# Performance work log

Measured on AMD Instinct MI355X. Metric: run time of the kernel, lower is better.

Reference implementation:

```python
import jax, jax.numpy as jnp
import numpy as np

N, E, D, H, O = 50000, 600000, 128, 128, 64


def _glorot(key, shape):
    fan_in, fan_out = shape[-1], shape[0]
    lim = (6.0 / (fan_in + fan_out)) ** 0.5
    return jax.random.uniform(key, shape, jnp.float32, -lim, lim)


def setup_inputs() -> dict:
    key = jax.random.key(0)
    ks = jax.random.split(key, 20)
    inp = {
        'x': jax.random.normal(ks[0], (N, D), dtype=jnp.float32),
        'edge_index': jax.random.randint(ks[1], (2, E), 0, N, dtype=jnp.int32),
        # FastLocalConv params
        'fl_W': _glorot(ks[2], (H, D)),
        'fl_b': jnp.zeros((H,), jnp.float32),
        'fl_att': _glorot(ks[3], (1, H)),
        # GIN layer 1 MLP: Linear(H,H) -> ReLU -> Linear(H,H)
        'g1_W1': _glorot(ks[4], (H, H)), 'g1_b1': jnp.zeros((H,), jnp.float32),
        'g1_W2': _glorot(ks[5], (H, H)), 'g1_b2': jnp.zeros((H,), jnp.float32),
        # GIN layer 2 MLP
        'g2_W1': _glorot(ks[6], (H, H)), 'g2_b1': jnp.zeros((H,), jnp.float32),
        'g2_W2': _glorot(ks[7], (H, H)), 'g2_b2': jnp.zeros((H,), jnp.float32),
        # output head
        'out_W': _glorot(ks[8], (O, H)), 'out_b': jnp.zeros((O,), jnp.float32),
    }
    return inp


def _fast_local(x, edge_index, W, b, att):
    # add self loops
    loops = jnp.arange(N, dtype=edge_index.dtype)
    row = jnp.concatenate([edge_index[0], loops])
    col = jnp.concatenate([edge_index[1], loops])
    h = x @ W.T + b                                   # [N,H]
    alpha = jax.nn.leaky_relu((h[row] * att[0]).sum(-1), 0.2)  # [E+N]
    # scatter-softmax grouped by source node (row), as in original code
    m = jax.ops.segment_max(alpha, row, num_segments=N)
    ea = jnp.exp(alpha - m[row])
    s = jax.ops.segment_sum(ea, row, num_segments=N)
    a = ea / s[row]
    # aggr='add' into target nodes (col), message = alpha * x_j (x_j = h[row])
    return jax.ops.segment_sum(a[:, None] * h[row], col, num_segments=N)


def _gin(h, edge_index, W1, b1, W2, b2):
    # GINConv (eps=0): mlp(x + sum_{j in N(i)} x_j), no self loops
    agg = jax.ops.segment_sum(h[edge_index[0]], edge_index[1], num_segments=N)
    z = h + agg
    z = jax.nn.relu(z @ W1.T + b1)
    return z @ W2.T + b2


def reference(x, edge_index, fl_W, fl_b, fl_att,
              g1_W1, g1_b1, g1_W2, g1_b2,
              g2_W1, g2_b1, g2_W2, g2_b2,
              out_W, out_b):
    h = _fast_local(x, edge_index, fl_W, fl_b, fl_att)
    h = jax.nn.relu(h)  # (dropout is eval no-op)
    h = jax.nn.relu(_gin(h, edge_index, g1_W1, g1_b1, g1_W2, g1_b2))
    h = jax.nn.relu(_gin(h, edge_index, g2_W1, g2_b1, g2_W2, g2_b2))
    logits = h @ out_W.T + out_b
    return jax.nn.log_softmax(logits, axis=1)
```

## Files before the change

### kernel.cpp

```cpp
#include <hip/hip_runtime.h>
#include <stdint.h>

typedef __attribute__((ext_vector_type(8))) short short8;
typedef __attribute__((ext_vector_type(4))) float floatx4;

#define HB 64
#define NMAX 50000
#define HW 12500

__device__ inline unsigned short f2bf(float f) {
  union { float f; unsigned int u; } v; v.f = f;
  unsigned int u = v.u;
  unsigned int r = (u + 0x7FFFu + ((u >> 16) & 1u)) >> 16;
  return (unsigned short)r;
}
__device__ inline unsigned int pk2(float a, float b) {
  return (unsigned int)f2bf(a) | ((unsigned int)f2bf(b) << 16);
}
template <bool RELU>
__device__ inline void acc8(uint4 u, float* a) {
  float f0 = __uint_as_float(u.x << 16), f1 = __uint_as_float(u.x & 0xffff0000u);
  float f2 = __uint_as_float(u.y << 16), f3 = __uint_as_float(u.y & 0xffff0000u);
  float f4 = __uint_as_float(u.z << 16), f5 = __uint_as_float(u.z & 0xffff0000u);
  float f6 = __uint_as_float(u.w << 16), f7 = __uint_as_float(u.w & 0xffff0000u);
  if (RELU) {
    f0 = fmaxf(f0, 0.f); f1 = fmaxf(f1, 0.f); f2 = fmaxf(f2, 0.f); f3 = fmaxf(f3, 0.f);
    f4 = fmaxf(f4, 0.f); f5 = fmaxf(f5, 0.f); f6 = fmaxf(f6, 0.f); f7 = fmaxf(f7, 0.f);
  }
  a[0] += f0; a[1] += f1; a[2] += f2; a[3] += f3;
  a[4] += f4; a[5] += f5; a[6] += f6; a[7] += f7;
}
__device__ inline uint4 pk8(const float* a) {
  uint4 p;
  p.x = pk2(a[0], a[1]); p.y = pk2(a[2], a[3]);
  p.z = pk2(a[4], a[5]); p.w = pk2(a[6], a[7]);
  return p;
}

__global__ __launch_bounds__(1024) void k_hist(const int* __restrict__ esrc,
                                               const int* __restrict__ edst,
                                               int E, int per,
                                               unsigned int* __restrict__ pAll) {
  __shared__ unsigned int h[HW];
  for (int i = threadIdx.x; i < HW; i += 1024) h[i] = 0;
  __syncthreads();
  const int* idx = blockIdx.y ? esrc : edst;
  int s = blockIdx.x * per, e = min(E, s + per);
  for (int j = s + threadIdx.x; j < e; j += 1024) {
    unsigned int d = (unsigned int)idx[j];
    atomicAdd(&h[d >> 2], 1u << ((d & 3) * 8));
  }
  __syncthreads();
  unsigned int* p = pAll + ((size_t)blockIdx.y * HB + blockIdx.x) * HW;
  for (int i = threadIdx.x; i < HW; i += 1024) p[i] = h[i];
}

__global__ __launch_bounds__(256) void k_reduce(unsigned int* __restrict__ pAll,
                                                int* __restrict__ deg,
                                                float* __restrict__ invc, int N) {
  int w = blockIdx.x * 256 + threadIdx.x;
  if (w >= HW) return;
  unsigned int* pd = pAll + w;
  const unsigned int* ps = pAll + (size_t)HB * HW + w;
  unsigned int r0 = 0, r1 = 0, r2 = 0, r3 = 0;
  for (int b = 0; b < HB; ++b) {
    unsigned int v = pd[(size_t)b * HW];
    pd[(size_t)b * HW] = r0 | (r1 << 8) | (r2 << 16) | (r3 << 24);
    r0 += v & 255u; r1 += (v >> 8) & 255u; r2 += (v >> 16) & 255u; r3 += v >> 24;
  }
  unsigned int s0 = 0, s1 = 0, s2 = 0, s3 = 0;
  for (int b = 0; b < HB; ++b) {
    unsigned int v = ps[(size_t)b * HW];
    s0 += v & 255u; s1 += (v >> 8) & 255u; s2 += (v >> 16) & 255u; s3 += v >> 24;
  }
  int n0 = 4 * w;
  unsigned int rr[4] = {r0, r1, r2, r3}, ss[4] = {s0, s1, s2, s3};
#pragma unroll
  for (int c = 0; c < 4; ++c) {
    if (n0 + c < N) {
      deg[n0 + c] = (int)rr[c];
      invc[n0 + c] = 1.0f / (1.0f + (float)ss[c]);
    }
  }
}

__global__ __launch_bounds__(1024) void k_scan_local(const int* __restrict__ deg,
                                                     int* __restrict__ off,
                                                     int* __restrict__ bsum, int N) {
  __shared__ int sb[1024];
  int tid = threadIdx.x;
  int i = blockIdx.x * 1024 + tid;
  int v = (i < N) ? deg[i] : 0;
  sb[tid] = v;
  __syncthreads();
  for (int d = 1; d < 1024; d <<= 1) {
    int t = (tid >= d) ? sb[tid - d] : 0;
    __syncthreads();
    sb[tid] += t;
    __syncthreads();
  }
  if (i < N) off[i] = sb[tid] - v;
  if (tid == 1023) bsum[blockIdx.x] = sb[1023];
}

__global__ __launch_bounds__(256) void k_scan_fix(int* off, const int* __restrict__ bsum,
                                                  int N, int E) {
  int i = blockIdx.x * 256 + threadIdx.x;
  if (i >= N) return;
  int nb = i >> 10;
  int s = 0;
  for (int c = 0; c < nb; ++c) s += bsum[c];
  off[i] += s;
  if (i == 0) off[N] = E;
}

__global__ __launch_bounds__(1024) void k_fill2(const int* __restrict__ esrc,
                                                const int* __restrict__ edst,
                                                int E, int per,
                                                const unsigned int* __restrict__ pAll,
                                                const int* __restrict__ off,
                                                int* __restrict__ srcs) {
  __shared__ unsigned int rk[HW];
  for (int i = threadIdx.x; i < HW; i += 1024) rk[i] = 0;
  __syncthreads();
  const unsigned int* slab = pAll + (size_t)blockIdx.x * HW;
  int s = blockIdx.x * per, e = min(E, s + per);
  for (int j = s + threadIdx.x; j < e; j += 1024) {
    unsigned int d = (unsigned int)edst[j];
    int sh = (d & 3) * 8;
    unsigned int rank = (atomicAdd(&rk[d >> 2], 1u << sh) >> sh) & 255u;
    unsigned int base = (slab[d >> 2] >> sh) & 255u;
    srcs[off[d] + (int)base + (int)rank] = esrc[j];
  }
}

__global__ __launch_bounds__(256) void k_gemm_fl(const float* __restrict__ in,
                                                 const float* __restrict__ W,
                                                 const float* __restrict__ bias,
                                                 const float* __restrict__ scale,
                                                 unsigned short* __restrict__ out, int N) {
  __shared__ unsigned short sx[64 * 136];
  __shared__ unsigned short sw[128 * 136];
  const int tid = threadIdx.x;
  const int nb = blockIdx.x * 64;

  for (int i = tid; i < 128 * 32; i += 256) {
    int h = i >> 5, k4 = i & 31;
    float4 wv = ((const float4*)W)[i];
    *(uint2*)&sw[h * 136 + k4 * 4] = make_uint2(pk2(wv.x, wv.y), pk2(wv.z, wv.w));
  }
  for (int i = tid; i < 64 * 32; i += 256) {
    int n = i >> 5, k4 = i & 31;
    int gn = nb + n;
    float4 xv;
    if (gn < N) xv = ((const float4*)in)[(size_t)gn * 32 + k4];
    else { xv.x = 0.f; xv.y = 0.f; xv.z = 0.f; xv.w = 0.f; }
    *(uint2*)&sx[n * 136 + k4 * 4] = make_uint2(pk2(xv.x, xv.y), pk2(xv.z, xv.w));
  }
  __syncthreads();

  const int wave = tid >> 6, lane = tid & 63;
  const int quad = lane >> 4, lq = lane & 15;
  floatx4 acc[8];
#pragma unroll
  for (int t = 0; t < 8; ++t) acc[t] = (floatx4){0.f, 0.f, 0.f, 0.f};
  const int arow = (wave * 16 + lq) * 136;
#pragma unroll
  for (int kt = 0; kt < 4; ++kt) {
    short8 a = *(const short8*)&sx[arow + kt * 32 + quad * 8];
#pragma unroll
    for (int t = 0; t < 8; ++t) {
      short8 b = *(const short8*)&sw[(t * 16 + lq) * 136 + kt * 32 + quad * 8];
      acc[t] = __builtin_amdgcn_mfma_f32_16x16x32_bf16(a, b, acc[t], 0, 0, 0);
    }
  }
#pragma unroll
  for (int t = 0; t < 8; ++t) {
    int h = t * 16 + lq;
    float bv = bias[h];
#pragma unroll
    for (int r = 0; r < 4; ++r) {
      int n = nb + wave * 16 + quad * 4 + r;
      if (n < N) out[(size_t)n * 128 + h] = f2bf((acc[t][r] + bv) * scale[n]);
    }
  }
}

__global__ __launch_bounds__(256) void k_agg_fl(const unsigned int* __restrict__ G,
                                                unsigned int* __restrict__ out,
                                                const int* __restrict__ off,
                                                const int* __restrict__ srcs, int N) {
  int n = (blockIdx.x * 256 + threadIdx.x) >> 4;
  if (n >= N) return;
  int l = threadIdx.x & 15;
  float a[8] = {0, 0, 0, 0, 0, 0, 0, 0};
  acc8<false>(((const uint4*)G)[(size_t)n * 16 + l], a);
  int s = off[n], e = off[n + 1];
  int j = s;
  for (; j + 4 <= e; j += 4) {
    int s0 = srcs[j], s1 = srcs[j + 1], s2 = srcs[j + 2], s3 = srcs[j + 3];
    uint4 u0 = ((const uint4*)G)[(size_t)s0 * 16 + l];
    uint4 u1 = ((const uint4*)G)[(size_t)s1 * 16 + l];
    uint4 u2 = ((const uint4*)G)[(size_t)s2 * 16 + l];
    uint4 u3 = ((const uint4*)G)[(size_t)s3 * 16 + l];
    acc8<false>(u0, a); acc8<false>(u1, a); acc8<false>(u2, a); acc8<false>(u3, a);
  }
  for (; j < e; ++j) acc8<false>(((const uint4*)G)[(size_t)srcs[j] * 16 + l], a);
  ((uint4*)out)[(size_t)n * 16 + l] = pk8(a);
}

__global__ __launch_bounds__(256) void k_gin(const unsigned int* __restrict__ G,
                                             const int* __restrict__ off,
                                             const int* __restrict__ srcs,
                                             const float* __restrict__ W1,
                                             const float* __restrict__ b1,
                                             const float* __restrict__ W2,
                                             const float* __restrict__ b2,
                                             unsigned short* __restrict__ out, int N) {
  __shared__ unsigned short sx[64 * 136];
  __shared__ unsigned short sw[128 * 136];
  const int tid = threadIdx.x;
  const int nb = blockIdx.x * 64;

  for (int i = tid; i < 128 * 32; i += 256) {
    int h = i >> 5, k4 = i & 31;
    float4 wv = ((const float4*)W1)[i];
    *(uint2*)&sw[h * 136 + k4 * 4] = make_uint2(pk2(wv.x, wv.y), pk2(wv.z, wv.w));
  }
  {
    int g = tid >> 4, l = tid & 15;
#pragma unroll
    for (int c = 0; c < 4; ++c) {
      int nloc = g * 4 + c;
      int n = nb + nloc;
      float a[8] = {0, 0, 0, 0, 0, 0, 0, 0};
      if (n < N) {
        acc8<true>(((const uint4*)G)[(size_t)n * 16 + l], a);
        int s = off[n], e = off[n + 1];
        int j = s;
        for (; j + 4 <= e; j += 4) {
          int s0 = srcs[j], s1 = srcs[j + 1], s2 = srcs[j + 2], s3 = srcs[j + 3];
          uint4 u0 = ((const uint4*)G)[(size_t)s0 * 16 + l];
          uint4 u1 = ((const uint4*)G)[(size_t)s1 * 16 + l];
          uint4 u2 = ((const uint4*)G)[(size_t)s2 * 16 + l];
          uint4 u3 = ((const uint4*)G)[(size_t)s3 * 16 + l];
          acc8<true>(u0, a); acc8<true>(u1, a); acc8<true>(u2, a); acc8<true>(u3, a);
        }
        for (; j < e; ++j) acc8<true>(((const uint4*)G)[(size_t)srcs[j] * 16 + l], a);
      }
      *(uint4*)&sx[nloc * 136 + l * 8] = pk8(a);
    }
  }
  __syncthreads();

  const int wave = tid >> 6, lane = tid & 63;
  const int quad = lane >> 4, lq = lane & 15;
  const int arow = (wave * 16 + lq) * 136;

  floatx4 acc[8];
#pragma unroll
  for (int t = 0; t < 8; ++t) acc[t] = (floatx4){0.f, 0.f, 0.f, 0.f};
#pragma unroll
  for (int kt = 0; kt < 4; ++kt) {
    short8 a = *(const short8*)&sx[arow + kt * 32 + quad * 8];
#pragma unroll
    for (int t = 0; t < 8; ++t) {
      short8 b = *(const short8*)&sw[(t * 16 + lq) * 136 + kt * 32 + quad * 8];
      acc[t] = __builtin_amdgcn_mfma_f32_16x16x32_bf16(a, b, acc[t], 0, 0, 0);
    }
  }
  __syncthreads();

#pragma unroll
  for (int t = 0; t < 8; ++t) {
    int h = t * 16 + lq;
    float bv = b1[h];
#pragma unroll
    for (int r = 0; r < 4; ++r) {
      int row = wave * 16 + quad * 4 + r;
      sx[row * 136 + h] = f2bf(fmaxf(acc[t][r] + bv, 0.f));
    }
  }
  for (int i = tid; i < 128 * 32; i += 256) {
    int h = i >> 5, k4 = i & 31;
    float4 wv = ((const float4*)W2)[i];
    *(uint2*)&sw[h * 136 + k4 * 4] = make_uint2(pk2(wv.x, wv.y), pk2(wv.z, wv.w));
  }
  __syncthreads();

#pragma unroll
  for (int t = 0; t < 8; ++t) acc[t] = (floatx4){0.f, 0.f, 0.f, 0.f};
#pragma unroll
  for (int kt = 0; kt < 4; ++kt) {
    short8 a = *(const short8*)&sx[arow + kt * 32 + quad * 8];
#pragma unroll
    for (int t = 0; t < 8; ++t) {
      short8 b = *(const short8*)&sw[(t * 16 + lq) * 136 + kt * 32 + quad * 8];
      acc[t] = __builtin_amdgcn_mfma_f32_16x16x32_bf16(a, b, acc[t], 0, 0, 0);
    }
  }
#pragma unroll
  for (int t = 0; t < 8; ++t) {
    int h = t * 16 + lq;
    float bv = b2[h];
#pragma unroll
    for (int r = 0; r < 4; ++r) {
      int n = nb + wave * 16 + quad * 4 + r;
      if (n < N) out[(size_t)n * 128 + h] = f2bf(acc[t][r] + bv);
    }
  }
}

__global__ __launch_bounds__(256) void k_gemm_head(const unsigned short* __restrict__ in,
                                                   const float* __restrict__ W,
                                                   const float* __restrict__ bias,
                                                   float* __restrict__ out, int N) {
  __shared__ unsigned short sx[64 * 136];
  __shared__ unsigned short sw[64 * 136];
  const int tid = threadIdx.x;
  const int nb = blockIdx.x * 64;

  for (int i = tid; i < 64 * 32; i += 256) {
    int h = i >> 5, k4 = i & 31;
    float4 wv = ((const float4*)W)[i];
    *(uint2*)&sw[h * 136 + k4 * 4] = make_uint2(pk2(wv.x, wv.y), pk2(wv.z, wv.w));
  }
  for (int i = tid; i < 64 * 16; i += 256) {
    int n = i >> 4, c = i & 15;
    int gn = nb + n;
    short8 t;
    if (gn < N) {
      t = *(const short8*)(in + (size_t)gn * 128 + c * 8);
#pragma unroll
      for (int q = 0; q < 8; ++q) {
        unsigned short u = (unsigned short)t[q];
        t[q] = (short)((u & 0x8000u) ? 0 : u);
      }
    } else t = (short8){0, 0, 0, 0, 0, 0, 0, 0};
    *(short8*)&sx[n * 136 + c * 8] = t;
  }
  __syncthreads();

  const int wave = tid >> 6, lane = tid & 63;
  const int quad = lane >> 4, lq = lane & 15;
  floatx4 acc[4];
#pragma unroll
  for (int t = 0; t < 4; ++t) acc[t] = (floatx4){0.f, 0.f, 0.f, 0.f};
  const int arow = (wave * 16 + lq) * 136;
#pragma unroll
  for (int kt = 0; kt < 4; ++kt) {
    short8 a = *(const short8*)&sx[arow + kt * 32 + quad * 8];
#pragma unroll
    for (int t = 0; t < 4; ++t) {
      short8 b = *(const short8*)&sw[(t * 16 + lq) * 136 + kt * 32 + quad * 8];
      acc[t] = __builtin_amdgcn_mfma_f32_16x16x32_bf16(a, b, acc[t], 0, 0, 0);
    }
  }
  float v[4][4];
#pragma unroll
  for (int t = 0; t < 4; ++t) {
    float bv = bias[t * 16 + lq];
#pragma unroll
    for (int r = 0; r < 4; ++r) v[t][r] = acc[t][r] + bv;
  }
#pragma unroll
  for (int r = 0; r < 4; ++r) {
    float m = fmaxf(fmaxf(v[0][r], v[1][r]), fmaxf(v[2][r], v[3][r]));
    m = fmaxf(m, __shfl_xor(m, 1));
    m = fmaxf(m, __shfl_xor(m, 2));
    m = fmaxf(m, __shfl_xor(m, 4));
    m = fmaxf(m, __shfl_xor(m, 8));
    float s = expf(v[0][r] - m) + expf(v[1][r] - m) + expf(v[2][r] - m) + expf(v[3][r] - m);
    s += __shfl_xor(s, 1);
    s += __shfl_xor(s, 2);
    s += __shfl_xor(s, 4);
    s += __shfl_xor(s, 8);
    float l = m + logf(s);
    int n = nb + wave * 16 + quad * 4 + r;
    if (n < N) {
#pragma unroll
      for (int t = 0; t < 4; ++t) out[(size_t)n * 64 + t * 16 + lq] = v[t][r] - l;
    }
  }
}

extern "C" void kernel_launch(void* const* d_in, const int* in_sizes, int n_in,
                              void* d_out, int out_size, void* d_ws, size_t ws_size,
                              hipStream_t stream) {
  const float* x     = (const float*)d_in[0];
  const int*   edges = (const int*)  d_in[1];
  const float* fl_W  = (const float*)d_in[2];
  const float* fl_b  = (const float*)d_in[3];
  const float* g1_W1 = (const float*)d_in[5];
  const float* g1_b1 = (const float*)d_in[6];
  const float* g1_W2 = (const float*)d_in[7];
  const float* g1_b2 = (const float*)d_in[8];
  const float* g2_W1 = (const float*)d_in[9];
  const float* g2_b1 = (const float*)d_in[10];
  const float* g2_W2 = (const float*)d_in[11];
  const float* g2_b2 = (const float*)d_in[12];
  const float* out_W = (const float*)d_in[13];
  const float* out_b = (const float*)d_in[14];

  const int N = in_sizes[0] / 128;
  const int E = in_sizes[1] / 2;
  const int* esrc = edges;
  const int* edst = edges + E;

  char* w = (char*)d_ws;
  unsigned short* A = (unsigned short*)w;  w += (size_t)N * 128 * 2;
  unsigned short* B = (unsigned short*)w;  w += (size_t)N * 128 * 2;
  int* deg    = (int*)w;   w += (size_t)N * 4;
  int* off    = (int*)w;   w += (size_t)(N + 1) * 4;
  float* invc = (float*)w; w += (size_t)N * 4;
  int* bsum   = (int*)w;   w += 1024 * 4;
  int* srcs   = (int*)w;   w += (size_t)E * 4;
  unsigned int* pAll = (unsigned int*)w; w += (size_t)2 * HB * HW * 4;

  const int GB = (N + 63) / 64;
  const int nchunk = (N + 1023) / 1024;
  const int per = (E + HB - 1) / HB;

  k_hist<<<dim3(HB, 2), 1024, 0, stream>>>(esrc, edst, E, per, pAll);
  k_reduce<<<(HW + 255) / 256, 256, 0, stream>>>(pAll, deg, invc, N);
  k_scan_local<<<nchunk, 1024, 0, stream>>>(deg, off, bsum, N);
  k_scan_fix<<<(N + 255) / 256, 256, 0, stream>>>(off, bsum, N, E);
  k_fill2<<<HB, 1024, 0, stream>>>(esrc, edst, E, per, pAll, off, srcs);

  k_gemm_fl<<<GB, 256, 0, stream>>>(x, fl_W, fl_b, invc, A, N);
  k_agg_fl<<<(N + 15) / 16, 256, 0, stream>>>((const unsigned int*)A, (unsigned int*)B, off, srcs, N);

  k_gin<<<GB, 256, 0, stream>>>((const unsigned int*)B, off, srcs, g1_W1, g1_b1, g1_W2, g1_b2, A, N);
  k_gin<<<GB, 256, 0, stream>>>((const unsigned int*)A, off, srcs, g2_W1, g2_b1, g2_W2, g2_b2, B, N);

  k_gemm_head<<<GB, 256, 0, stream>>>(B, out_W, out_b, (float*)d_out, N);
}
```

Measured before the change: 336.3 us.

## Split GIN aggregation from MLP, preconvert weights to bf16 once

The fused GIN kernel, where each 64-node block gathered neighbours with only 256 threads before its GEMM, is split into a standalone high-parallelism aggregation kernel (16 threads per node over the whole grid) followed by a separate MLP GEMM kernel. ReLU is moved into the aggregation output and the MLP epilogue rather than applied per gathered element. All weight matrices are converted to bf16 by a small kernel at the start, so GEMM blocks copy bf16 weights directly instead of converting fp32 per block. The cost is an extra intermediate buffer, an extra global round trip of the aggregated features, and more kernel launches.

Measured after the change: 295.5 us, median of 2. 1.14x faster.

```diff
diff --git a/kernel.cpp b/kernel.cpp
--- a/kernel.cpp
+++ b/kernel.cpp
@@ -5,7 +5,6 @@
 typedef __attribute__((ext_vector_type(4))) float floatx4;
 
 #define HB 64
-#define NMAX 50000
 #define HW 12500
 
 __device__ inline unsigned short f2bf(float f) {
@@ -17,24 +16,32 @@
 __device__ inline unsigned int pk2(float a, float b) {
   return (unsigned int)f2bf(a) | ((unsigned int)f2bf(b) << 16);
 }
-template <bool RELU>
 __device__ inline void acc8(uint4 u, float* a) {
-  float f0 = __uint_as_float(u.x << 16), f1 = __uint_as_float(u.x & 0xffff0000u);
-  float f2 = __uint_as_float(u.y << 16), f3 = __uint_as_float(u.y & 0xffff0000u);
-  float f4 = __uint_as_float(u.z << 16), f5 = __uint_as_float(u.z & 0xffff0000u);
-  float f6 = __uint_as_float(u.w << 16), f7 = __uint_as_float(u.w & 0xffff0000u);
-  if (RELU) {
-    f0 = fmaxf(f0, 0.f); f1 = fmaxf(f1, 0.f); f2 = fmaxf(f2, 0.f); f3 = fmaxf(f3, 0.f);
-    f4 = fmaxf(f4, 0.f); f5 = fmaxf(f5, 0.f); f6 = fmaxf(f6, 0.f); f7 = fmaxf(f7, 0.f);
-  }
-  a[0] += f0; a[1] += f1; a[2] += f2; a[3] += f3;
-  a[4] += f4; a[5] += f5; a[6] += f6; a[7] += f7;
+  a[0] += __uint_as_float(u.x << 16); a[1] += __uint_as_float(u.x & 0xffff0000u);
+  a[2] += __uint_as_float(u.y << 16); a[3] += __uint_as_float(u.y & 0xffff0000u);
+  a[4] += __uint_as_float(u.z << 16); a[5] += __uint_as_float(u.z & 0xffff0000u);
+  a[6] += __uint_as_float(u.w << 16); a[7] += __uint_as_float(u.w & 0xffff0000u);
 }
 __device__ inline uint4 pk8(const float* a) {
   uint4 p;
   p.x = pk2(a[0], a[1]); p.y = pk2(a[2], a[3]);
   p.z = pk2(a[4], a[5]); p.w = pk2(a[6], a[7]);
   return p;
+}
+
+__global__ __launch_bounds__(256) void k_wconv(const float* __restrict__ s0, const float* __restrict__ s1,
+                                               const float* __restrict__ s2, const float* __restrict__ s3,
+                                               const float* __restrict__ s4, const float* __restrict__ s5,
+                                               unsigned short* __restrict__ dst) {
+  int b = blockIdx.x;
+  int seg = b >> 4;
+  int rel = b & 15;
+  const float* sp[6] = {s0, s1, s2, s3, s4, s5};
+  const float* src = sp[seg];
+  int i = rel * 1024 + threadIdx.x * 4;
+  float4 v = *(const float4*)(src + i);
+  size_t o = (size_t)seg * 16384 + i;
+  *(uint2*)(dst + o) = make_uint2(pk2(v.x, v.y), pk2(v.z, v.w));
 }
 
 __global__ __launch_bounds__(1024) void k_hist(const int* __restrict__ esrc,
@@ -135,7 +142,7 @@
 }
 
 __global__ __launch_bounds__(256) void k_gemm_fl(const float* __restrict__ in,
-                                                 const float* __restrict__ W,
+                                                 const unsigned short* __restrict__ Wb,
                                                  const float* __restrict__ bias,
                                                  const float* __restrict__ scale,
                                                  unsigned short* __restrict__ out, int N) {
@@ -144,10 +151,9 @@
   const int tid = threadIdx.x;
   const int nb = blockIdx.x * 64;
 
-  for (int i = tid; i < 128 * 32; i += 256) {
-    int h = i >> 5, k4 = i & 31;
-    float4 wv = ((const float4*)W)[i];
-    *(uint2*)&sw[h * 136 + k4 * 4] = make_uint2(pk2(wv.x, wv.y), pk2(wv.z, wv.w));
+  for (int i = tid; i < 128 * 16; i += 256) {
+    int h = i >> 4, c = i & 15;
+    *(short8*)&sw[h * 136 + c * 8] = ((const short8*)Wb)[i];
   }
   for (int i = tid; i < 64 * 32; i += 256) {
     int n = i >> 5, k4 = i & 31;
@@ -186,35 +192,38 @@
   }
 }
 
-__global__ __launch_bounds__(256) void k_agg_fl(const unsigned int* __restrict__ G,
-                                                unsigned int* __restrict__ out,
-                                                const int* __restrict__ off,
-                                                const int* __restrict__ srcs, int N) {
+template <bool RELU_OUT>
+__global__ __launch_bounds__(256) void k_agg(const uint4* __restrict__ G,
+                                             uint4* __restrict__ out,
+                                             const int* __restrict__ off,
+                                             const int* __restrict__ srcs, int N) {
   int n = (blockIdx.x * 256 + threadIdx.x) >> 4;
   if (n >= N) return;
   int l = threadIdx.x & 15;
   float a[8] = {0, 0, 0, 0, 0, 0, 0, 0};
-  acc8<false>(((const uint4*)G)[(size_t)n * 16 + l], a);
+  acc8(G[(size_t)n * 16 + l], a);
   int s = off[n], e = off[n + 1];
   int j = s;
   for (; j + 4 <= e; j += 4) {
     int s0 = srcs[j], s1 = srcs[j + 1], s2 = srcs[j + 2], s3 = srcs[j + 3];
-    uint4 u0 = ((const uint4*)G)[(size_t)s0 * 16 + l];
-    uint4 u1 = ((const uint4*)G)[(size_t)s1 * 16 + l];
-    uint4 u2 = ((const uint4*)G)[(size_t)s2 * 16 + l];
-    uint4 u3 = ((const uint4*)G)[(size_t)s3 * 16 + l];
-    acc8<false>(u0, a); acc8<false>(u1, a); acc8<false>(u2, a); acc8<false>(u3, a);
-  }
-  for (; j < e; ++j) acc8<false>(((const uint4*)G)[(size_t)srcs[j] * 16 + l], a);
-  ((uint4*)out)[(size_t)n * 16 + l] = pk8(a);
-}
-
-__global__ __launch_bounds__(256) void k_gin(const unsigned int* __restrict__ G,
-                                             const int* __restrict__ off,
-                                             const int* __restrict__ srcs,
-                                             const float* __restrict__ W1,
+    uint4 u0 = G[(size_t)s0 * 16 + l];
+    uint4 u1 = G[(size_t)s1 * 16 + l];
+    uint4 u2 = G[(size_t)s2 * 16 + l];
+    uint4 u3 = G[(size_t)s3 * 16 + l];
+    acc8(u0, a); acc8(u1, a); acc8(u2, a); acc8(u3, a);
+  }
+  for (; j < e; ++j) acc8(G[(size_t)srcs[j] * 16 + l], a);
+  if (RELU_OUT) {
+#pragma unroll
+    for (int q = 0; q < 8; ++q) a[q] = fmaxf(a[q], 0.f);
+  }
+  out[(size_t)n * 16 + l] = pk8(a);
+}
+
+__global__ __launch_bounds__(256) void k_mlp(const unsigned short* __restrict__ in,
+                                             const unsigned short* __restrict__ W1b,
                                              const float* __restrict__ b1,
-                                             const float* __restrict__ W2,
+                                             const unsigned short* __restrict__ W2b,
                                              const float* __restrict__ b2,
                                              unsigned short* __restrict__ out, int N) {
   __shared__ unsigned short sx[64 * 136];
@@ -222,34 +231,17 @@
   const int tid = threadIdx.x;
   const int nb = blockIdx.x * 64;
 
-  for (int i = tid; i < 128 * 32; i += 256) {
-    int h = i >> 5, k4 = i & 31;
-    float4 wv = ((const float4*)W1)[i];
-    *(uint2*)&sw[h * 136 + k4 * 4] = make_uint2(pk2(wv.x, wv.y), pk2(wv.z, wv.w));
-  }
-  {
-    int g = tid >> 4, l = tid & 15;
-#pragma unroll
-    for (int c = 0; c < 4; ++c) {
-      int nloc = g * 4 + c;
-      int n = nb + nloc;
-      float a[8] = {0, 0, 0, 0, 0, 0, 0, 0};
-      if (n < N) {
-        acc8<true>(((const uint4*)G)[(size_t)n * 16 + l], a);
-        int s = off[n], e = off[n + 1];
-        int j = s;
-        for (; j + 4 <= e; j += 4) {
-          int s0 = srcs[j], s1 = srcs[j + 1], s2 = srcs[j + 2], s3 = srcs[j + 3];
-          uint4 u0 = ((const uint4*)G)[(size_t)s0 * 16 + l];
-          uint4 u1 = ((const uint4*)G)[(size_t)s1 * 16 + l];
-          uint4 u2 = ((const uint4*)G)[(size_t)s2 * 16 + l];
-          uint4 u3 = ((const uint4*)G)[(size_t)s3 * 16 + l];
-          acc8<true>(u0, a); acc8<true>(u1, a); acc8<true>(u2, a); acc8<true>(u3, a);
-        }
-        for (; j < e; ++j) acc8<true>(((const uint4*)G)[(size_t)srcs[j] * 16 + l], a);
-      }
-      *(uint4*)&sx[nloc * 136 + l * 8] = pk8(a);
-    }
+  for (int i = tid; i < 128 * 16; i += 256) {
+    int h = i >> 4, c = i & 15;
+    *(short8*)&sw[h * 136 + c * 8] = ((const short8*)W1b)[i];
+  }
+  for (int i = tid; i < 64 * 16; i += 256) {
+    int n = i >> 4, c = i & 15;
+    int gn = nb + n;
+    short8 t;
+    if (gn < N) t = *(const short8*)(in + (size_t)gn * 128 + c * 8);
+    else t = (short8){0, 0, 0, 0, 0, 0, 0, 0};
+    *(short8*)&sx[n * 136 + c * 8] = t;
   }
   __syncthreads();
 
@@ -281,10 +273,9 @@
       sx[row * 136 + h] = f2bf(fmaxf(acc[t][r] + bv, 0.f));
     }
   }
-  for (int i = tid; i < 128 * 32; i += 256) {
-    int h = i >> 5, k4 = i & 31;
-    float4 wv = ((const float4*)W2)[i];
-    *(uint2*)&sw[h * 136 + k4 * 4] = make_uint2(pk2(wv.x, wv.y), pk2(wv.z, wv.w));
+  for (int i = tid; i < 128 * 16; i += 256) {
+    int h = i >> 4, c = i & 15;
+    *(short8*)&sw[h * 136 + c * 8] = ((const short8*)W2b)[i];
   }
   __syncthreads();
 
@@ -306,37 +297,30 @@
 #pragma unroll
     for (int r = 0; r < 4; ++r) {
       int n = nb + wave * 16 + quad * 4 + r;
-      if (n < N) out[(size_t)n * 128 + h] = f2bf(acc[t][r] + bv);
-    }
-  }
-}
-
-__global__ __launch_bounds__(256) void k_gemm_head(const unsigned short* __restrict__ in,
-                                                   const float* __restrict__ W,
-                                                   const float* __restrict__ bias,
-                                                   float* __restrict__ out, int N) {
+      if (n < N) out[(size_t)n * 128 + h] = f2bf(fmaxf(acc[t][r] + bv, 0.f));
+    }
+  }
+}
+
+__global__ __launch_bounds__(256) void k_head(const unsigned short* __restrict__ in,
+                                              const unsigned short* __restrict__ Wb,
+                                              const float* __restrict__ bias,
+                                              float* __restrict__ out, int N) {
   __shared__ unsigned short sx[64 * 136];
   __shared__ unsigned short sw[64 * 136];
   const int tid = threadIdx.x;
   const int nb = blockIdx.x * 64;
 
-  for (int i = tid; i < 64 * 32; i += 256) {
-    int h = i >> 5, k4 = i & 31;
-    float4 wv = ((const float4*)W)[i];
-    *(uint2*)&sw[h * 136 + k4 * 4] = make_uint2(pk2(wv.x, wv.y), pk2(wv.z, wv.w));
+  for (int i = tid; i < 64 * 16; i += 256) {
+    int h = i >> 4, c = i & 15;
+    *(short8*)&sw[h * 136 + c * 8] = ((const short8*)Wb)[i];
   }
   for (int i = tid; i < 64 * 16; i += 256) {
     int n = i >> 4, c = i & 15;
     int gn = nb + n;
     short8 t;
-    if (gn < N) {
-      t = *(const short8*)(in + (size_t)gn * 128 + c * 8);
-#pragma unroll
-      for (int q = 0; q < 8; ++q) {
-        unsigned short u = (unsigned short)t[q];
-        t[q] = (short)((u & 0x8000u) ? 0 : u);
-      }
-    } else t = (short8){0, 0, 0, 0, 0, 0, 0, 0};
+    if (gn < N) t = *(const short8*)(in + (size_t)gn * 128 + c * 8);
+    else t = (short8){0, 0, 0, 0, 0, 0, 0, 0};
     *(short8*)&sx[n * 136 + c * 8] = t;
   }
   __syncthreads();
@@ -410,6 +394,8 @@
   char* w = (char*)d_ws;
   unsigned short* A = (unsigned short*)w;  w += (size_t)N * 128 * 2;
   unsigned short* B = (unsigned short*)w;  w += (size_t)N * 128 * 2;
+  unsigned short* C = (unsigned short*)w;  w += (size_t)N * 128 * 2;
+  unsigned short* Wb = (unsigned short*)w; w += 90112 * 2;
   int* deg    = (int*)w;   w += (size_t)N * 4;
   int* off    = (int*)w;   w += (size_t)(N + 1) * 4;
   float* invc = (float*)w; w += (size_t)N * 4;
@@ -418,8 +404,11 @@
   unsigned int* pAll = (unsigned int*)w; w += (size_t)2 * HB * HW * 4;
 
   const int GB = (N + 63) / 64;
+  const int AGB = (N * 16 + 255) / 256;
   const int nchunk = (N + 1023) / 1024;
   const int per = (E + HB - 1) / HB;
+
+  k_wconv<<<88, 256, 0, stream>>>(fl_W, g1_W1, g1_W2, g2_W1, g2_W2, out_W, Wb);
 
   k_hist<<<dim3(HB, 2), 1024, 0, stream>>>(esrc, edst, E, per, pAll);
   k_reduce<<<(HW + 255) / 256, 256, 0, stream>>>(pAll, deg, invc, N);
@@ -427,11 +416,14 @@
   k_scan_fix<<<(N + 255) / 256, 256, 0, stream>>>(off, bsum, N, E);
   k_fill2<<<HB, 1024, 0, stream>>>(esrc, edst, E, per, pAll, off, srcs);
 
-  k_gemm_fl<<<GB, 256, 0, stream>>>(x, fl_W, fl_b, invc, A, N);
-  k_agg_fl<<<(N + 15) / 16, 256, 0, stream>>>((const unsigned int*)A, (unsigned int*)B, off, srcs, N);
-
-  k_gin<<<GB, 256, 0, stream>>>((const unsigned int*)B, off, srcs, g1_W1, g1_b1, g1_W2, g1_b2, A, N);
-  k_gin<<<GB, 256, 0, stream>>>((const unsigned int*)A, off, srcs, g2_W1, g2_b1, g2_W2, g2_b2, B, N);
-
-  k_gemm_head<<<GB, 256, 0, stream>>>(B, out_W, out_b, (float*)d_out, N);
-}
+  k_gemm_fl<<<GB, 256, 0, stream>>>(x, Wb, fl_b, invc, A, N);
+  k_agg<true><<<AGB, 256, 0, stream>>>((const uint4*)A, (uint4*)B, off, srcs, N);
+
+  k_agg<false><<<AGB, 256, 0, stream>>>((const uint4*)B, (uint4*)C, off, srcs, N);
+  k_mlp<<<GB, 256, 0, stream>>>(C, Wb + 16384, g1_b1, Wb + 32768, g1_b2, A, N);
+
+  k_agg<false><<<AGB, 256, 0, stream>>>((const uint4*)A, (uint4*)C, off, srcs, N);
+  k_mlp<<<GB, 256, 0, stream>>>(C, Wb + 49152, g2_b1, Wb + 65536, g2_b2, B, N);
+
+  k_head<<<GB, 256, 0, stream>>>(B, Wb + 81920, out_b, (float*)d_out, N);
+}
```
